# Kernel optimization log

Hardware: AMD Instinct MI355X
Metric: run time of the kernel (lower is better)

The kernel has to match this reference:

```python
import jax, jax.numpy as jnp
import numpy as np

N, M, KNN, KUP, POS_DIM = 15872, 35637, 5, 20, 32


def _pos_emb_table(n, d):
    # transformer-style sinusoidal table (matches PosEmb._define_pos_emb)
    pos = np.arange(n, dtype=np.float32)[:, None]
    i2 = np.arange(0, d, 2, dtype=np.float32)
    div = 10000.0 ** (i2 / d)
    pe = np.zeros((n, d), dtype=np.float32)
    pe[:, 0::2] = np.sin(pos / div)
    pe[:, 1::2] = np.cos(pos / div)
    return jnp.asarray(pe)


def _lrelu(x):
    return jnp.where(x > 0, x, 0.2 * x)


def _gather(x, idx):
    # x: [B,n,d], idx: [B,m,k] -> [B,m,k,d]
    return jax.vmap(lambda xb, ib: xb[ib])(x, idx)


def _knn_idx(x, k):
    # x: [B,n,d]; k nearest excluding self (torch knn drops column 0 of topk)
    xx = jnp.sum(x * x, axis=-1)
    neg = 2.0 * jnp.einsum('bnd,bmd->bnm', x, x) - xx[:, :, None] - xx[:, None, :]
    _, idx = jax.lax.top_k(neg, k + 1)
    return idx[..., 1:]


def _emb_block(feat, idx, ec_w1, ec_s1, ec_h1, ec_w2, ec_b2,
               w1, s1, h1, w2, s2, h2, w3, s3, h3, w4, b4):
    # get_graph_feature: [B,n,k,2*in] = cat(nbr - ctr, ctr)
    nbr = _gather(feat, idx)
    ctr = jnp.broadcast_to(feat[:, :, None, :], nbr.shape)
    e = jnp.concatenate([nbr - ctr, ctr], axis=-1)
    # edge_conv (1x1 conv2d = per-edge linear); BN folded into scale/shift (eval mode)
    e = _lrelu(jnp.einsum('bnkc,oc->bnko', e, ec_w1) * ec_s1 + ec_h1)
    e = jnp.einsum('bnkc,oc->bnko', e, ec_w2) + ec_b2
    f1 = jnp.max(e, axis=2)                                   # max over k neighbors -> [B,n,out]
    fmax = jnp.broadcast_to(jnp.max(f1, axis=1, keepdims=True), f1.shape)
    favg = jnp.broadcast_to(jnp.mean(f1, axis=1, keepdims=True), f1.shape)
    h = jnp.concatenate([feat, f1, fmax, favg], axis=-1)      # [B,n,3*out+in]
    # fc_out: 1x1 conv1d stack = per-point MLP with folded BN + LeakyReLU
    h = _lrelu(h @ w1.T * s1 + h1)
    h = _lrelu(h @ w2.T * s2 + h2)
    h = _lrelu(h @ w3.T * s3 + h3)
    return h @ w4.T + b4


def _forward(lx, ldx, pos_emb,
             b0_ec_w1, b0_ec_s1, b0_ec_h1, b0_ec_w2, b0_ec_b2,
             b0_fc_w1, b0_fc_s1, b0_fc_h1, b0_fc_w2, b0_fc_s2, b0_fc_h2,
             b0_fc_w3, b0_fc_s3, b0_fc_h3, b0_fc_w4, b0_fc_b4,
             b1_ec_w1, b1_ec_s1, b1_ec_h1, b1_ec_w2, b1_ec_b2,
             b1_fc_w1, b1_fc_s1, b1_fc_h1, b1_fc_w2, b1_fc_s2, b1_fc_h2,
             b1_fc_w3, b1_fc_s3, b1_fc_h3, b1_fc_w4, b1_fc_b4,
             up_inputs, up_w0, up_s0, up_h0, up_w_rest, up_s_rest, up_h_rest, up_wf, up_bf,
             dec_w0, dec_b0, dec_w1, dec_b1, dec_w2, dec_b2, dec_w3, dec_b3,
             dec_w4, dec_b4, dec_wf, dec_bf,
             idx0, up_idx):
    B = ldx.shape[0]
    feat_in = jnp.concatenate([ldx, jnp.broadcast_to(pos_emb[None], (B,) + pos_emb.shape)], axis=-1)  # [B,N,35]
    f0 = _emb_block(feat_in, idx0,
                    b0_ec_w1, b0_ec_s1, b0_ec_h1, b0_ec_w2, b0_ec_b2,
                    b0_fc_w1, b0_fc_s1, b0_fc_h1, b0_fc_w2, b0_fc_s2, b0_fc_h2,
                    b0_fc_w3, b0_fc_s3, b0_fc_h3, b0_fc_w4, b0_fc_b4)   # [B,N,64]
    idx1 = _knn_idx(f0, KNN)                                            # dynamic feature-space KNN
    f1 = _emb_block(f0, idx1,
                    b1_ec_w1, b1_ec_s1, b1_ec_h1, b1_ec_w2, b1_ec_b2,
                    b1_fc_w1, b1_fc_s1, b1_fc_h1, b1_fc_w2, b1_fc_s2, b1_fc_h2,
                    b1_fc_w3, b1_fc_s3, b1_fc_h3, b1_fc_w4, b1_fc_b4)   # [B,N,128]
    x_feat = jnp.concatenate([feat_in, f0, f1], axis=-1)                # [B,N,227]
    # Upscale: SIREN-activated 1x1-conv stack -> softmax interpolation weights over KUP lo-res nbrs
    h = jnp.sin(jnp.einsum('bmkc,oc->bmko', up_inputs[:B], up_w0) * up_s0 + up_h0)
    for i in range(up_w_rest.shape[0]):
        h = jnp.sin(jnp.einsum('bmkc,oc->bmko', h, up_w_rest[i]) * up_s_rest[i] + up_h_rest[i])
    logits = jnp.einsum('bmkc,oc->bmko', h, up_wf) + up_bf              # [B,M,KUP,1]
    w = jax.nn.softmax(logits, axis=2)
    grouped = _gather(x_feat, up_idx)                                   # [B,M,KUP,227]
    z = jnp.sum(w * grouped, axis=2)                                    # [B,M,227]
    # SIREN decoder: dims [227,256,128,64,32,16,3]; zip with 5 mods applies first 5 layers + head
    h = jnp.sin(30.0 * (z @ dec_w0.T + dec_b0))
    h = jnp.sin(h @ dec_w1.T + dec_b1)
    h = jnp.sin(h @ dec_w2.T + dec_b2)
    h = jnp.sin(h @ dec_w3.T + dec_b3)
    h = jnp.sin(h @ dec_w4.T + dec_b4)
    return h @ dec_wf.T + dec_bf                                        # [B,M,3]


def setup_inputs():
    key = jax.random.key(0)
    ks = iter(jax.random.split(key, 100))
    def rn(*s):
        return jax.random.normal(next(ks), s, jnp.float32) * 0.05
    def sc(*s):
        return jax.random.uniform(next(ks), s, jnp.float32, minval=0.5, maxval=1.5)
    inp = {}
    inp['lx'] = jax.random.normal(next(ks), (1, N, 3), jnp.float32)
    inp['ldx'] = jax.random.normal(next(ks), (1, N, 3), jnp.float32)
    inp['pos_emb'] = _pos_emb_table(N, POS_DIM)
    inp['idx0'] = jax.random.randint(next(ks), (1, N, KNN), 0, N - 1)
    # EmbModule 0: in=35, out=64
    inp['b0_ec_w1'], inp['b0_ec_s1'], inp['b0_ec_h1'] = rn(128, 70), sc(128), rn(128)
    inp['b0_ec_w2'], inp['b0_ec_b2'] = rn(64, 128), rn(64)
    inp['b0_fc_w1'], inp['b0_fc_s1'], inp['b0_fc_h1'] = rn(192, 227), sc(192), rn(192)
    inp['b0_fc_w2'], inp['b0_fc_s2'], inp['b0_fc_h2'] = rn(128, 192), sc(128), rn(128)
    inp['b0_fc_w3'], inp['b0_fc_s3'], inp['b0_fc_h3'] = rn(64, 128), sc(64), rn(64)
    inp['b0_fc_w4'], inp['b0_fc_b4'] = rn(64, 64), rn(64)
    # EmbModule 1: in=64, out=128
    inp['b1_ec_w1'], inp['b1_ec_s1'], inp['b1_ec_h1'] = rn(256, 128), sc(256), rn(256)
    inp['b1_ec_w2'], inp['b1_ec_b2'] = rn(128, 256), rn(128)
    inp['b1_fc_w1'], inp['b1_fc_s1'], inp['b1_fc_h1'] = rn(384, 448), sc(384), rn(384)
    inp['b1_fc_w2'], inp['b1_fc_s2'], inp['b1_fc_h2'] = rn(256, 384), sc(256), rn(256)
    inp['b1_fc_w3'], inp['b1_fc_s3'], inp['b1_fc_h3'] = rn(128, 256), sc(128), rn(128)
    inp['b1_fc_w4'], inp['b1_fc_b4'] = rn(128, 128), rn(128)
    inp['up_inputs'] = jax.random.uniform(next(ks), (1, M, KUP, 7), jnp.float32)
    inp['up_idx'] = jax.random.randint(next(ks), (1, M, KUP), 0, N - 1)
    inp['up_w0'], inp['up_s0'], inp['up_h0'] = rn(128, 7), sc(128), rn(128)
    inp['up_w_rest'], inp['up_s_rest'], inp['up_h_rest'] = rn(7, 128, 128), sc(7, 128), rn(7, 128)
    inp['up_wf'], inp['up_bf'] = rn(1, 128), rn(1)
    # SIREN decoder
    dd = [227, 256, 128, 64, 32, 16]
    for i in range(5):
        inp['dec_w%d' % i], inp['dec_b%d' % i] = rn(dd[i + 1], dd[i]), rn(dd[i + 1])
    inp['dec_wf'], inp['dec_bf'] = rn(3, 16), rn(3)
    return inp


def reference(lx, ldx, pos_emb, idx0,
              b0_ec_w1, b0_ec_s1, b0_ec_h1, b0_ec_w2, b0_ec_b2,
              b0_fc_w1, b0_fc_s1, b0_fc_h1, b0_fc_w2, b0_fc_s2, b0_fc_h2,
              b0_fc_w3, b0_fc_s3, b0_fc_h3, b0_fc_w4, b0_fc_b4,
              b1_ec_w1, b1_ec_s1, b1_ec_h1, b1_ec_w2, b1_ec_b2,
              b1_fc_w1, b1_fc_s1, b1_fc_h1, b1_fc_w2, b1_fc_s2, b1_fc_h2,
              b1_fc_w3, b1_fc_s3, b1_fc_h3, b1_fc_w4, b1_fc_b4,
              up_inputs, up_idx, up_w0, up_s0, up_h0,
              up_w_rest, up_s_rest, up_h_rest, up_wf, up_bf,
              dec_w0, dec_b0, dec_w1, dec_b1, dec_w2, dec_b2, dec_w3, dec_b3,
              dec_w4, dec_b4, dec_wf, dec_bf):
    return _forward(lx, ldx, pos_emb,
                    b0_ec_w1, b0_ec_s1, b0_ec_h1, b0_ec_w2, b0_ec_b2,
                    b0_fc_w1, b0_fc_s1, b0_fc_h1, b0_fc_w2, b0_fc_s2, b0_fc_h2,
                    b0_fc_w3, b0_fc_s3, b0_fc_h3, b0_fc_w4, b0_fc_b4,
                    b1_ec_w1, b1_ec_s1, b1_ec_h1, b1_ec_w2, b1_ec_b2,
                    b1_fc_w1, b1_fc_s1, b1_fc_h1, b1_fc_w2, b1_fc_s2, b1_fc_h2,
                    b1_fc_w3, b1_fc_s3, b1_fc_h3, b1_fc_w4, b1_fc_b4,
                    up_inputs, up_w0, up_s0, up_h0, up_w_rest, up_s_rest, up_h_rest, up_wf, up_bf,
                    dec_w0, dec_b0, dec_w1, dec_b1, dec_w2, dec_b2, dec_w3, dec_b3,
                    dec_w4, dec_b4, dec_wf, dec_bf,
                    idx0, up_idx)
```

## Files before the change

kernel.cpp:

```cpp
#include <hip/hip_runtime.h>
#include <hip/hip_bf16.h>
#include <math.h>

#define N_PTS 15872
#define M_PTS 35637
#define KNN_K 5
#define KUP   20
#define UP_ROWS (M_PTS * KUP)
#define NTILE (N_PTS/32)
#define N_EDGE (N_PTS*KNN_K)
#define CDIV(a,b) (((a)+(b)-1)/(b))

typedef __hip_bfloat16 bf16;
typedef unsigned int uint;
typedef unsigned short ushort_t;
__device__ __forceinline__ float b2f(bf16 x){ return __bfloat162float(x); }

__device__ __forceinline__ uint f2bf_bits(float x){
  uint u = __float_as_uint(x);
  return (u + 0x7FFFu + ((u>>16)&1u)) >> 16;
}

__device__ __forceinline__ ushort_t f2h_bits(float x){
  union { _Float16 h; ushort_t u; } c; c.h = (_Float16)x; return c.u;
}

typedef __attribute__((ext_vector_type(8))) short bf16x8;
typedef __attribute__((ext_vector_type(8))) _Float16 f16x8;
typedef __attribute__((ext_vector_type(2))) __fp16 fp16x2_t;
typedef __attribute__((ext_vector_type(16))) float f32x16;
union FragAB { bf16x8 v; uint u[4]; };
union FragB  { bf16x8 v; uint4 q; };
union FragH  { f16x8 v; uint4 q; _Float16 h[8]; };
union Acc16  { f32x16 v; float f[16]; };
union H2U    { fp16x2_t h; uint u; };

__global__ void flag_k(const uint* __restrict__ pos_raw, int* __restrict__ flag){
  if (threadIdx.x == 0 && blockIdx.x == 0)
    flag[0] = (pos_raw[0] == 0x3F800000u) ? 1 : 0;
}

struct CvtTab { const void* src[52]; int start[52]; };
__global__ __launch_bounds__(256) void cvt_all_k(CvtTab tab, float* __restrict__ dst,
                                                 const int* __restrict__ flag, int total){
  int i = blockIdx.x*256 + threadIdx.x;
  if (i >= total) return;
  int s = 0;
#pragma unroll 1
  for (int k = 1; k < 52; k++) if (tab.start[k] <= i) s = k;
  int off = i - tab.start[s];
  float v = flag[0] ? b2f(((const bf16*)tab.src[s])[off]) : ((const float*)tab.src[s])[off];
  dst[i] = v;
}

__global__ void packfrag16_k(const float* __restrict__ w, const float* __restrict__ sr,
                             ushort_t* __restrict__ out, int n){
  int i = blockIdx.x*256 + threadIdx.x;
  if (i >= n) return;
  int j = i & 7;
  int lam = (i >> 3) & 63;
  int fg = i >> 9;
  int t = fg & 3, ks = (fg >> 2) & 1, Q = (fg >> 3) & 3, l = fg >> 5;
  int nn = t*32 + (lam & 31);
  int kk = Q*32 + ks*16 + ((j>>2)<<3) + ((lam>>5)<<2) + (j&3);
  float x = w[l*16384 + nn*128 + kk] * sr[l*128 + nn];
  out[i] = f2h_bits(x);
}

__global__ void packw_mfma_k(const float* __restrict__ w, ushort_t* __restrict__ whi,
                             ushort_t* __restrict__ wlo, int N, int K, int ldk,
                             int Kpad, int total){
  int i = blockIdx.x*256 + threadIdx.x;
  if (i >= total) return;
  int j = i & 7;
  int lane = (i >> 3) & 63;
  int fr = i >> 9;
  int nq = Kpad >> 5;
  int ks = fr & 1;
  int q  = (fr >> 1) % nq;
  int nt = (fr >> 1) / nq;
  int n = nt*32 + (lane & 31);
  int k = q*32 + ks*16 + (lane >> 5)*8 + j;
  float x = (n < N && k < K) ? w[(size_t)n*ldk + k] : 0.f;
  uint hb = f2bf_bits(x);
  uint lb = f2bf_bits(x - __uint_as_float(hb << 16));
  whi[i] = (ushort_t)hb;
  wlo[i] = (ushort_t)lb;
}

__global__ void packknn_k(const float* __restrict__ xf, const float* __restrict__ nr,
                          ushort_t* __restrict__ ahi, ushort_t* __restrict__ alo,
                          ushort_t* __restrict__ bhi, ushort_t* __restrict__ blo){
  int i = blockIdx.x*256 + threadIdx.x;
  if (i >= NTILE*5*64*8) return;
  int e = i & 7;
  int lane = (i >> 3) & 63;
  int rest = i >> 9;
  int kc = rest % 5, jt = rest / 5;
  int n = jt*32 + (lane & 31);
  int k = kc*16 + (lane >> 5)*8 + e;
  float f = (k < 64) ? xf[(size_t)n*227 + 35 + k] : 0.f;
  float av, bv;
  if (k < 64)      { av = 2.f*f;   bv = f; }
  else if (k == 64){ av = nr[n];   bv = -1.f; }
  else if (k == 65){ av = 1.f;     bv = -nr[n]; }
  else             { av = 0.f;     bv = 0.f; }
  uint ah = f2bf_bits(av); uint al = f2bf_bits(av - __uint_as_float(ah<<16));
  uint bh = f2bf_bits(bv); uint bl = f2bf_bits(bv - __uint_as_float(bh<<16));
  ahi[i] = (ushort_t)ah; alo[i] = (ushort_t)al;
  bhi[i] = (ushort_t)bh; blo[i] = (ushort_t)bl;
}

__global__ void fillmark_k(bf16* __restrict__ out, int n){
  int i = blockIdx.x*256 + threadIdx.x;
  if (i < n) out[i] = __float2bfloat16(12345.0f);
}

__global__ void foldshift_k(const float* __restrict__ W, int ldw,
                            int off1, int C1, const float* __restrict__ v1,
                            int off2, int C2, const float* __restrict__ v2,
                            const float* __restrict__ scale, const float* __restrict__ shift,
                            float* __restrict__ out, int N){
  int n = blockIdx.x*256 + threadIdx.x;
  if (n >= N) return;
  const float* wr = W + (size_t)n*ldw;
  float s = 0.f;
  for (int j=0;j<C1;j++) s += wr[off1+j]*v1[j];
  for (int j=0;j<C2;j++) s += wr[off2+j]*v2[j];
  out[n] = s*scale[n] + shift[n];
}

template<int EPI, int ACT>
__global__ __launch_bounds__(256) void gemm_k(
    const float* __restrict__ A, int lda,
    const float* __restrict__ W, int ldw,
    const float* __restrict__ scale, const float* __restrict__ shift,
    float gmul, float* __restrict__ C, int ldc,
    int M, int Nout, int K)
{
  __shared__ __align__(16) float As[16][64];
  __shared__ __align__(16) float Ws[16][64];
  const int tid = threadIdx.x;
  const int tx = tid & 15, ty = tid >> 4;
  const int bm = blockIdx.x * 64, bn = blockIdx.y * 64;
  const int ar = tid >> 2, ak = (tid & 3) * 4;
  float acc[4][4] = {};
  for (int k0 = 0; k0 < K; k0 += 16) {
    float a0=0.f,a1=0.f,a2=0.f,a3=0.f;
    int grow = bm + ar;
    if (grow < M) {
      const float* ap = A + (size_t)grow * lda + (k0 + ak);
      int rem = K - (k0 + ak);
      if (rem >= 4) { a0=ap[0]; a1=ap[1]; a2=ap[2]; a3=ap[3]; }
      else { if(rem>0)a0=ap[0]; if(rem>1)a1=ap[1]; if(rem>2)a2=ap[2]; }
    }
    float w0=0.f,w1=0.f,w2=0.f,w3=0.f;
    int gn = bn + ar;
    if (gn < Nout) {
      const float* wp = W + (size_t)gn * ldw + (k0 + ak);
      int rem = K - (k0 + ak);
      if (rem >= 4) { w0=wp[0]; w1=wp[1]; w2=wp[2]; w3=wp[3]; }
      else { if(rem>0)w0=wp[0]; if(rem>1)w1=wp[1]; if(rem>2)w2=wp[2]; }
    }
    __syncthreads();
    As[ak+0][ar]=a0; As[ak+1][ar]=a1; As[ak+2][ar]=a2; As[ak+3][ar]=a3;
    Ws[ak+0][ar]=w0; Ws[ak+1][ar]=w1; Ws[ak+2][ar]=w2; Ws[ak+3][ar]=w3;
    __syncthreads();
#pragma unroll
    for (int kk = 0; kk < 16; kk++) {
      float4 av = *reinterpret_cast<const float4*>(&As[kk][ty*4]);
      float4 wv = *reinterpret_cast<const float4*>(&Ws[kk][tx*4]);
      float aa[4] = {av.x,av.y,av.z,av.w};
      float ww[4] = {wv.x,wv.y,wv.z,wv.w};
#pragma unroll
      for (int i=0;i<4;i++)
#pragma unroll
        for (int j=0;j<4;j++) acc[i][j] += aa[i]*ww[j];
    }
  }
#pragma unroll
  for (int i=0;i<4;i++){
    int m = bm + ty*4 + i;
    if (m >= M) continue;
#pragma unroll
    for (int j=0;j<4;j++){
      int n = bn + tx*4 + j;
      if (n >= Nout) continue;
      float v = acc[i][j];
      if (EPI==0)      v = v * scale[n] + shift[n];
      else if (EPI==1) v = v + shift[n];
      else             v = (v + shift[n]) * gmul;
      if (ACT==1)      v = v > 0.f ? v : 0.2f*v;
      else if (ACT==2) v = sinf(v);
      C[(size_t)m*ldc + n] = v;
    }
  }
}

struct MLayer { int K, N, Kq, Nt, woff, soff, hoff, epi, act; float gmul; };
struct MCfg { MLayer L[6]; };

template<int NL, int OUTMODE>
__global__ __launch_bounds__(256) void mlp_fused_k(
    const float* __restrict__ A0, int lda0, int K0, int M,
    MCfg cfg,
    const ushort_t* __restrict__ wh, const ushort_t* __restrict__ wl,
    const float* __restrict__ wc,
    float* __restrict__ Cout, int ldc,
    void* __restrict__ oflg, const int* __restrict__ flag)
{
  __shared__ __align__(16) uint slab[64*256];
  const int tid = threadIdx.x;
  const int lane = tid & 63;
  const int wv = tid >> 6;
  const int np = lane & 31;
  const int hb2 = lane >> 5;
  const int rhalf = wv & 1, thalf = wv >> 1;
  const int rb = blockIdx.x * 64;
  const int row_l = rhalf*32 + np;

  for (int e = tid; e < 64*64; e += 256) {
    int r = e >> 6, g = e & 63;
    int gr = rb + r;
    uint p[4];
#pragma unroll
    for (int u=0;u<4;u++){
      int k = g*4+u;
      float f = (gr < M && k < K0) ? A0[(size_t)gr*lda0 + k] : 0.f;
      uint hb = f2bf_bits(f);
      uint lb = f2bf_bits(f - __uint_as_float(hb<<16));
      p[u] = (hb<<16) | lb;
    }
    *(uint4*)&slab[r*256 + (((g ^ r) & 63)<<2)] = make_uint4(p[0],p[1],p[2],p[3]);
  }
  __syncthreads();

#pragma unroll 1
  for (int l = 0; l < NL; l++){
    const int N = cfg.L[l].N, Kq = cfg.L[l].Kq, Nt = cfg.L[l].Nt;
    const int woff = cfg.L[l].woff, soff = cfg.L[l].soff, hoff = cfg.L[l].hoff;
    const int epi = cfg.L[l].epi, actf = cfg.L[l].act;
    const float gmul = cfg.L[l].gmul;
    Acc16 acc[4];
#pragma unroll
    for (int u=0;u<4;u++)
#pragma unroll
      for (int i=0;i<16;i++) acc[u].f[i] = 0.f;

#pragma unroll 1
    for (int q = 0; q < Kq; q++){
#pragma unroll
      for (int ks = 0; ks < 2; ks++){
        int g0 = (q*32 + ks*16 + hb2*8) >> 2;
        uint4 a0 = *(const uint4*)&slab[row_l*256 + ((((g0  ) ^ row_l) & 63)<<2)];
        uint4 a1 = *(const uint4*)&slab[row_l*256 + ((((g0+1) ^ row_l) & 63)<<2)];
        uint au[8] = {a0.x,a0.y,a0.z,a0.w,a1.x,a1.y,a1.z,a1.w};
        FragAB ah, al;
#pragma unroll
        for (int p=0;p<4;p++){
          ah.u[p] = (au[2*p]>>16)     | (au[2*p+1] & 0xFFFF0000u);
          al.u[p] = (au[2*p]&0xFFFFu) | (au[2*p+1]<<16);
        }
#pragma unroll
        for (int u=0;u<4;u++){
          int t = thalf + u*2;
          if (t < Nt){
            size_t fb = (size_t)woff + ((size_t)((t*Kq + q)*2 + ks))*512 + (size_t)lane*8;
            FragB bh, bl;
            bh.q = *(const uint4*)(wh + fb);
            bl.q = *(const uint4*)(wl + fb);
            acc[u].v = __builtin_amdgcn_mfma_f32_32x32x16_bf16(ah.v, bh.v, acc[u].v, 0,0,0);
            acc[u].v = __builtin_amdgcn_mfma_f32_32x32x16_bf16(al.v, bh.v, acc[u].v, 0,0,0);
            acc[u].v = __builtin_amdgcn_mfma_f32_32x32x16_bf16(ah.v, bl.v, acc[u].v, 0,0,0);
          }
        }
      }
    }
    __syncthreads();
#pragma unroll
    for (int u=0;u<4;u++){
      int t = thalf + u*2;
      if (t < Nt){
        int col = t*32 + np;
        if (col < N){
          float scv = (epi==0) ? wc[soff+col] : 0.f;
          float shv = wc[hoff+col];
#pragma unroll
          for (int reg=0;reg<16;reg++){
            int r32 = (reg&3) + 8*(reg>>2) + 4*hb2;
            float v = acc[u].f[reg];
            if (epi==0)      v = v*scv + shv;
            else if (epi==1) v = v + shv;
            else             v = (v + shv)*gmul;
            if (actf==1)      v = v > 0.f ? v : 0.2f*v;
            else if (actf==2) v = __sinf(v);
            if (l == NL-1){
              int gr = rb + rhalf*32 + r32;
              if (gr < M){
                if (OUTMODE==0) Cout[(size_t)gr*ldc + col] = v;
                else {
                  if (!(fabsf(v) < 1e30f)) v = 777.0f;
                  size_t oi = (size_t)gr*3 + col;
                  if (flag[0]) ((bf16*)oflg)[oi] = __float2bfloat16(v);
                  else         ((float*)oflg)[oi] = v;
                }
              }
            } else {
              int r = rhalf*32 + r32;
              uint hb = f2bf_bits(v);
              uint lb = f2bf_bits(v - __uint_as_float(hb<<16));
              slab[r*256 + ((((col>>2) ^ r) & 63)<<2) + (col&3)] = (hb<<16) | lb;
            }
          }
        }
      }
    }
    __syncthreads();
  }
}

#define INS5(tv, tj, v, j) \
  if ((v) > tv[4]){ tv[4]=(v); tj[4]=(j); \
    _Pragma("unroll") \
    for (int q=4;q>0;q--) \
      if (tv[q] > tv[q-1]){ float tf=tv[q-1]; tv[q-1]=tv[q]; tv[q]=tf; \
                            int ti=tj[q-1]; tj[q-1]=tj[q]; tj[q]=ti; } }

__global__ __launch_bounds__(256) void knn_mfma_k(
    const ushort_t* __restrict__ ahi, const ushort_t* __restrict__ alo,
    const ushort_t* __restrict__ bhi, const ushort_t* __restrict__ blo,
    int* __restrict__ out)
{
  __shared__ float mv[4][32][5];
  __shared__ int   mjj[4][32][5];
  const int tid = threadIdx.x;
  const int lane = tid & 63;
  const int wv = tid >> 6;
  const int np = lane & 31;
  const int hb2 = lane >> 5;
  const int it = blockIdx.x;
  const int ig = it*32 + np;

  FragB vh[5], vl[5];
  {
    size_t bb = (size_t)(it*5)*512 + (size_t)lane*8;
#pragma unroll
    for (int kc=0;kc<5;kc++){
      vh[kc].q = *(const uint4*)(bhi + bb + kc*512);
      vl[kc].q = *(const uint4*)(blo + bb + kc*512);
    }
  }

  float tv[5] = {-1e30f,-1e30f,-1e30f,-1e30f,-1e30f};
  int   tj[5] = {0,0,0,0,0};

  FragB uh[5], ul[5], nh[5], nl[5];
  {
    size_t ab = (size_t)(wv*5)*512 + (size_t)lane*8;
#pragma unroll
    for (int kc=0;kc<5;kc++){
      uh[kc].q = *(const uint4*)(ahi + ab + kc*512);
      ul[kc].q = *(const uint4*)(alo + ab + kc*512);
    }
  }

#pragma unroll 1
  for (int t = 0; t < NTILE/4; t++){
    int jt = wv + t*4;
    if (t+1 < NTILE/4){
      size_t an = (size_t)((jt+4)*5)*512 + (size_t)lane*8;
#pragma unroll
      for (int kc=0;kc<5;kc++){
        nh[kc].q = *(const uint4*)(ahi + an + kc*512);
        nl[kc].q = *(const uint4*)(alo + an + kc*512);
      }
    }
    Acc16 acc;
#pragma unroll
    for (int q=0;q<16;q++) acc.f[q] = 0.f;
#pragma unroll
    for (int kc=0;kc<5;kc++){
      acc.v = __builtin_amdgcn_mfma_f32_32x32x16_bf16(uh[kc].v, vh[kc].v, acc.v, 0,0,0);
      acc.v = __builtin_amdgcn_mfma_f32_32x32x16_bf16(ul[kc].v, vh[kc].v, acc.v, 0,0,0);
      acc.v = __builtin_amdgcn_mfma_f32_32x32x16_bf16(uh[kc].v, vl[kc].v, acc.v, 0,0,0);
    }
    int jb = jt*32 + 4*hb2;
#pragma unroll
    for (int reg=0;reg<16;reg++){
      int j = jb + (reg&3) + 8*(reg>>2);
      float v = acc.f[reg];
      if (j != ig) { INS5(tv, tj, v, j); }
    }
    if (t+1 < NTILE/4){
#pragma unroll
      for (int kc=0;kc<5;kc++){ uh[kc] = nh[kc]; ul[kc] = nl[kc]; }
    }
  }

#pragma unroll
  for (int s=0;s<5;s++){
    float ov = __shfl_xor(tv[s], 32, 64);
    int   oj = __shfl_xor(tj[s], 32, 64);
    INS5(tv, tj, ov, oj);
  }
  if (hb2 == 0){
#pragma unroll
    for (int s=0;s<5;s++){ mv[wv][np][s] = tv[s]; mjj[wv][np][s] = tj[s]; }
  }
  __syncthreads();
  if (tid < 32){
    float bv[5]; int bj[5];
#pragma unroll
    for (int s=0;s<5;s++){ bv[s] = mv[0][tid][s]; bj[s] = mjj[0][tid][s]; }
#pragma unroll
    for (int w=1;w<4;w++)
#pragma unroll
      for (int s=0;s<5;s++){
        float v = mv[w][tid][s]; int j = mjj[w][tid][s];
        INS5(bv, bj, v, j);
      }
    int gi = it*32 + tid;
#pragma unroll
    for (int s=0;s<5;s++) out[gi*KNN_K + s] = bj[s];
  }
}

__global__ __launch_bounds__(256) void siren_fused_k(
    const void* __restrict__ upin,
    const ushort_t* __restrict__ wf16,
    const float* __restrict__ W0c, const float* __restrict__ S0c, const float* __restrict__ H0c,
    const float* __restrict__ HRc,
    const float* __restrict__ WFc, const float* __restrict__ BFc,
    float* __restrict__ logits, const int* __restrict__ flag)
{
  __shared__ float intile[4*32*8];
  __shared__ __align__(16) float w0s[128*8];
  __shared__ __align__(16) float hrs[7*128];
  __shared__ __align__(16) float wfs[128];
  __shared__ float bfs[1];

  const int tid  = threadIdx.x;
  const int lane = tid & 63;
  const int wv   = tid >> 6;
  const int np   = lane & 31;
  const int hb2  = lane >> 5;
  const int rowbase = blockIdx.x * 128 + wv * 32;
  const int isbf = flag[0];
  float* intw = intile + wv*32*8;

  for (int e = tid; e < 128*7; e += 256){
    int c = e/7, k = e%7;
    w0s[c*8+k] = W0c[e]*S0c[c];
  }
  if (tid < 128) w0s[tid*8+7] = H0c[tid];
  for (int e = tid; e < 7*128; e += 256) hrs[e] = HRc[e];
  if (tid < 128) wfs[tid] = WFc[tid];
  if (tid == 0) bfs[0] = BFc[0];
  for (int e = lane; e < 32*7; e += 64) {
    int r = e/7, k = e%7;
    int gr = rowbase + r;
    float v = 0.f;
    if (gr < UP_ROWS)
      v = isbf ? b2f(((const bf16*)upin)[(size_t)gr*7+k]) : ((const float*)upin)[(size_t)gr*7+k];
    intw[r*8+k] = v;
  }
  __syncthreads();

  uint st0[16], st1[16];
  {
    float xin[7];
#pragma unroll
    for (int k=0;k<7;k++) xin[k] = intw[np*8+k];
#pragma unroll
    for (int g = 0; g < 16; g++){
      float xs[4];
#pragma unroll
      for (int j = 0; j < 4; j++){
        int c = g*8 + hb2*4 + j;
        const float4 wa = *(const float4*)&w0s[c*8];
        const float4 wb = *(const float4*)&w0s[c*8+4];
        float a = wb.w;
        a += xin[0]*wa.x; a += xin[1]*wa.y; a += xin[2]*wa.z; a += xin[3]*wa.w;
        a += xin[4]*wb.x; a += xin[5]*wb.y; a += xin[6]*wb.z;
        xs[j] = __sinf(a);
      }
      H2U u0,u1;
      u0.h = __builtin_amdgcn_cvt_pkrtz(xs[0],xs[1]);
      u1.h = __builtin_amdgcn_cvt_pkrtz(xs[2],xs[3]);
      st0[g] = u0.u; st1[g] = u1.u;
    }
  }

  FragH fr[8];
#pragma unroll
  for (int m = 0; m < 8; m++)
    fr[m].q = make_uint4(st0[2*m], st1[2*m], st0[2*m+1], st1[2*m+1]);

  uint nst0[16], nst1[16];
#pragma unroll 1
  for (int l = 0; l < 7; l++) {
#pragma unroll
    for (int tp = 0; tp < 2; tp++){
      Acc16 acc0, acc1;
#pragma unroll
      for (int i=0;i<16;i++){ acc0.f[i] = 0.f; acc1.f[i] = 0.f; }
#pragma unroll
      for (int m = 0; m < 8; m++){
        int fb = (((l*8 + m)*4 + tp*2) << 9) + lane*8;
        FragH bh0, bh1;
        bh0.q = *(const uint4*)(wf16 + fb);
        bh1.q = *(const uint4*)(wf16 + fb + 512);
        acc0.v = __builtin_amdgcn_mfma_f32_32x32x16_f16(bh0.v, fr[m].v, acc0.v, 0,0,0);
        acc1.v = __builtin_amdgcn_mfma_f32_32x32x16_f16(bh1.v, fr[m].v, acc1.v, 0,0,0);
      }
#pragma unroll
      for (int rg = 0; rg < 4; rg++){
        int g0 = (tp*2+0)*4 + rg;
        const float4 b0v = *(const float4*)&hrs[l*128 + g0*8 + hb2*4];
        float x0 = __sinf(acc0.f[rg*4+0] + b0v.x);
        float x1 = __sinf(acc0.f[rg*4+1] + b0v.y);
        float x2 = __sinf(acc0.f[rg*4+2] + b0v.z);
        float x3 = __sinf(acc0.f[rg*4+3] + b0v.w);
        H2U u0,u1;
        u0.h = __builtin_amdgcn_cvt_pkrtz(x0,x1);
        u1.h = __builtin_amdgcn_cvt_pkrtz(x2,x3);
        nst0[g0] = u0.u; nst1[g0] = u1.u;

        int g1 = (tp*2+1)*4 + rg;
        const float4 b1v = *(const float4*)&hrs[l*128 + g1*8 + hb2*4];
        float y0 = __sinf(acc1.f[rg*4+0] + b1v.x);
        float y1 = __sinf(acc1.f[rg*4+1] + b1v.y);
        float y2 = __sinf(acc1.f[rg*4+2] + b1v.z);
        float y3 = __sinf(acc1.f[rg*4+3] + b1v.w);
        H2U v0,v1;
        v0.h = __builtin_amdgcn_cvt_pkrtz(y0,y1);
        v1.h = __builtin_amdgcn_cvt_pkrtz(y2,y3);
        nst0[g1] = v0.u; nst1[g1] = v1.u;
      }
    }
    if (l < 6){
#pragma unroll
      for (int m = 0; m < 8; m++)
        fr[m].q = make_uint4(nst0[2*m], nst1[2*m], nst0[2*m+1], nst1[2*m+1]);
    }
  }

  {
    float a = 0.f;
#pragma unroll
    for (int g = 0; g < 16; g++){
      const float4 w4 = *(const float4*)&wfs[g*8 + hb2*4];
      H2U u0,u1; u0.u = nst0[g]; u1.u = nst1[g];
      a += (float)u0.h.x*w4.x + (float)u0.h.y*w4.y
         + (float)u1.h.x*w4.z + (float)u1.h.y*w4.w;
    }
    a += __shfl_xor(a, 32, 64);
    int gr = rowbase + np;
    if (hb2 == 0 && gr < UP_ROWS) logits[gr] = a + bfs[0];
  }
}

__global__ void featin_k(const void* __restrict__ ldx, const void* __restrict__ pos,
                         float* __restrict__ xf, const int* __restrict__ flag){
  int i = blockIdx.x*256 + threadIdx.x;
  if (i >= N_PTS*35) return;
  int n = i / 35, c = i % 35;
  float v;
  if (flag[0]) {
    v = (c < 3) ? b2f(((const bf16*)ldx)[n*3+c]) : b2f(((const bf16*)pos)[n*32 + (c-3)]);
  } else {
    v = (c < 3) ? ((const float*)ldx)[n*3+c] : ((const float*)pos)[n*32 + (c-3)];
  }
  xf[(size_t)n*227 + c] = v;
}

__global__ void gather_e_k(const float* __restrict__ xf, int coff, int CIN,
                           const int* __restrict__ idx, float* __restrict__ e,
                           int n0, int np){
  int W2 = 2*CIN;
  int i = blockIdx.x*256 + threadIdx.x;
  if (i >= np*KNN_K*W2) return;
  int c = i % W2; int ek = i / W2;
  int nl = ek / KNN_K, k = ek % KNN_K;
  int n = n0 + nl;
  int j = idx[n*KNN_K + k];
  float out;
  if (c < CIN) out = xf[(size_t)j*227 + coff + c] - xf[(size_t)n*227 + coff + c];
  else         out = xf[(size_t)n*227 + coff + (c-CIN)];
  e[(size_t)ek*W2 + c] = out;
}

__global__ void kmax_k(const float* __restrict__ e2, int C, float* __restrict__ f1,
                       int n0, int np){
  int i = blockIdx.x*256 + threadIdx.x;
  if (i >= np*C) return;
  int nl = i / C, c = i % C;
  float v = -1e30f;
  for (int k=0;k<KNN_K;k++) v = fmaxf(v, e2[((size_t)nl*KNN_K+k)*C + c]);
  f1[(size_t)(n0+nl)*C + c] = v;
}

template<int C>
__global__ __launch_bounds__(256) void reduce1_k(const float* __restrict__ X, int n,
                                                 float* __restrict__ pmax, float* __restrict__ psum){
  const int tid = threadIdx.x;
  const int c = tid % C;
  const int r0 = tid / C;
  const int TPR = 256 / C;
  float vmax = -1e30f, vsum = 0.f;
  for (int row = blockIdx.x * TPR + r0; row < n; row += gridDim.x * TPR) {
    float v = X[(size_t)row * C + c];
    vmax = fmaxf(vmax, v); vsum += v;
  }
  __shared__ float smax[256], ssum[256];
  smax[tid]=vmax; ssum[tid]=vsum;
  __syncthreads();
  if (tid < C) {
    for (int q=1;q<TPR;q++){ vmax=fmaxf(vmax, smax[q*C+c]); vsum += ssum[q*C+c]; }
    pmax[blockIdx.x*C + c] = vmax; psum[blockIdx.x*C + c] = vsum;
  }
}

template<int C>
__global__ void reduce2_k(const float* __restrict__ pmax, const float* __restrict__ psum,
                          int nblk, float invn, float* __restrict__ fmaxo, float* __restrict__ favgo){
  int c = threadIdx.x; if (c >= C) return;
  float vmax=-1e30f, vsum=0.f;
  for (int b=0;b<nblk;b++){ vmax=fmaxf(vmax,pmax[b*C+c]); vsum+=psum[b*C+c]; }
  fmaxo[c]=vmax; favgo[c]=vsum*invn;
}

__global__ void concat_k(const float* __restrict__ xf, int coff, int CF,
                         const float* __restrict__ f1, int C,
                         const float* __restrict__ fmax, const float* __restrict__ favg,
                         float* __restrict__ h, int n0, int np){
  int W = CF + 3*C;
  int i = blockIdx.x*256 + threadIdx.x;
  if (i >= np*W) return;
  int nl = i / W, c = i % W;
  int n = n0 + nl;
  float v;
  if (c < CF)          v = xf[(size_t)n*227 + coff + c];
  else if (c < CF+C)   v = f1[(size_t)n*C + (c-CF)];
  else if (c < CF+2*C) v = fmax[c-CF-C];
  else                 v = favg[c-CF-2*C];
  h[(size_t)nl*W + c] = v;
}

__global__ void concat2_k(const float* __restrict__ xf, int coff, int CF,
                          const float* __restrict__ f1, int C,
                          float* __restrict__ h, int n0, int np){
  int W = CF + C;
  int i = blockIdx.x*256 + threadIdx.x;
  if (i >= np*W) return;
  int nl = i / W, c = i % W;
  int n = n0 + nl;
  float v = (c < CF) ? xf[(size_t)n*227 + coff + c] : f1[(size_t)n*C + (c-CF)];
  h[(size_t)nl*W + c] = v;
}

__global__ void norms_k(const float* __restrict__ xf, float* __restrict__ nr){
  int n = blockIdx.x*256 + threadIdx.x;
  if (n >= N_PTS) return;
  const float* p = xf + (size_t)n*227 + 35;
  float s = 0.f;
  for (int d=0;d<64;d++) s += p[d]*p[d];
  nr[n] = s;
}

__global__ __launch_bounds__(64) void softgather_k(const float* __restrict__ logits,
                                                   const int* __restrict__ up_idx,
                                                   const float* __restrict__ xf,
                                                   float* __restrict__ z){
  __shared__ float lw[KUP]; __shared__ int li[KUP];
  int m = blockIdx.x;
  int tid = threadIdx.x;
  if (tid < KUP){ lw[tid] = logits[(size_t)m*KUP + tid]; li[tid] = up_idx[(size_t)m*KUP + tid]; }
  __syncthreads();
  float mx = -1e30f;
  for (int k=0;k<KUP;k++) mx = fmaxf(mx, lw[k]);
  __syncthreads();
  if (tid < KUP) lw[tid] = expf(lw[tid]-mx);
  __syncthreads();
  float s = 0.f;
  for (int k=0;k<KUP;k++) s += lw[k];
  float inv = 1.f/s;
  for (int c = tid; c < 227; c += 64){
    float acc = 0.f;
    for (int k=0;k<KUP;k++) acc += lw[k] * xf[(size_t)li[k]*227 + c];
    z[(size_t)m*227 + c] = acc*inv;
  }
}

extern "C" void kernel_launch(void* const* d_in, const int* in_sizes, int n_in,
                              void* d_out, int out_size, void* d_ws, size_t ws_size,
                              hipStream_t stream) {
  const int *idx0  = (const int*)d_in[3];
  const int *upidx = (const int*)d_in[37];

  float* ws = (float*)d_ws;
  float* x_feat = ws;
  float* f1b    = ws + 3602944;
  float* pmax   = ws + 5634560;
  float* psum   = ws + 5667328;
  float* fmaxv  = ws + 5700096;
  float* favgv  = ws + 5700224;
  int*   flag   = (int*)(ws + 5700352);
  int*   idx1   = (int*)(ws + 5700368);
  float* nrm    = ws + 5779728;
  float* logits = ws + 5795600;
  float* wcvt   = ws + 6508352;
  float* S      = ws + 7214400;
  float* fold0  = S + 9500000;
  float* fold1  = S + 9500192;
  ushort_t* whi  = (ushort_t*)(S + 9662464);
  ushort_t* wlo  = whi + 114688;
  ushort_t* gwhi = wlo + 114688;
  ushort_t* gwlo = gwhi + 331776;

  const size_t NEED = (size_t)(7214400 + 9662464) * 4
                    + (size_t)(114688*2 + 331776*2) * 2;
  if (ws_size < NEED) {
    fillmark_k<<<CDIV(out_size,256),256,0,stream>>>((bf16*)d_out, out_size);
    return;
  }

  flag_k<<<1,64,0,stream>>>((const uint*)d_in[2], flag);
  CvtTab tab;
  int wcoff = 0, seg = 0;
  auto CVT = [&](int i, int n)->const float* {
    tab.src[seg] = d_in[i]; tab.start[seg] = wcoff; seg++;
    const float* p = wcvt + wcoff; wcoff += n;
    return p;
  };
  const float *E0W1=CVT(4,8960),  *E0S1=CVT(5,128),  *E0H1=CVT(6,128),
              *E0W2=CVT(7,8192),  *E0B2=CVT(8,64);
  const float *F0W1=CVT(9,43584), *F0S1=CVT(10,192), *F0H1=CVT(11,192),
              *F0W2=CVT(12,24576),*F0S2=CVT(13,128), *F0H2=CVT(14,128),
              *F0W3=CVT(15,8192), *F0S3=CVT(16,64),  *F0H3=CVT(17,64),
              *F0W4=CVT(18,4096), *F0B4=CVT(19,64);
  const float *E1W1=CVT(20,32768),*E1S1=CVT(21,256), *E1H1=CVT(22,256),
              *E1W2=CVT(23,32768),*E1B2=CVT(24,128);
  const float *F1W1=CVT(25,172032),*F1S1=CVT(26,384),*F1H1=CVT(27,384),
              *F1W2=CVT(28,98304),*F1S2=CVT(29,256), *F1H2=CVT(30,256),
              *F1W3=CVT(31,32768),*F1S3=CVT(32,128), *F1H3=CVT(33,128),
              *F1W4=CVT(34,16384),*F1B4=CVT(35,128);
  const float *UPW0=CVT(38,896),  *UPS0=CVT(39,128), *UPH0=CVT(40,128),
              *UPWR=CVT(41,114688),*UPSR=CVT(42,896),*UPHR=CVT(43,896),
              *UPWF=CVT(44,128),  *UPBF=CVT(45,1);
  const float *DW0=CVT(46,58112), *DB0=CVT(47,256),
              *DW1=CVT(48,32768), *DB1=CVT(49,128),
              *DW2=CVT(50,8192),  *DB2=CVT(51,64),
              *DW3=CVT(52,2048),  *DB3=CVT(53,32),
              *DW4=CVT(54,512),   *DB4=CVT(55,16),
              *DWF=CVT(56,48),    *DBF=CVT(57,3);
  cvt_all_k<<<CDIV(wcoff,256),256,0,stream>>>(tab, wcvt, flag, wcoff);

  packfrag16_k<<<CDIV(114688,256),256,0,stream>>>(UPWR, UPSR, whi, 114688);

  int offs[16]; const float* srcs[16]; int Ns[16], Ks[16], Ldk[16], Kps[16];
  {
    int o = 0, q = 0;
    auto REG = [&](const float* s, int N, int K, int ldk, int Kpad){
      srcs[q]=s; Ns[q]=N; Ks[q]=K; Ldk[q]=ldk; Kps[q]=Kpad; offs[q]=o;
      o += CDIV(N,32)*32*Kpad; q++;
    };
    REG(F0W1,192, 99,227,128);
    REG(F0W2,128,192,192,192); REG(F0W3,64,128,128,128); REG(F0W4,64,64,64,64);
    REG(DW0,256,227,227,256);  REG(DW1,128,256,256,256);  REG(DW2,64,128,128,128);
    REG(DW3,32,64,64,64);      REG(DW4,16,32,32,32);      REG(DWF,3,16,16,32);
    REG(E0W1,128,70,70,96);    REG(E0W2,64,128,128,128);
    REG(E1W1,256,128,128,128); REG(E1W2,128,256,256,256);
    REG(F1W3,128,256,256,256); REG(F1W4,128,128,128,128);
  }
  for (int q = 0; q < 16; q++){
    int total = CDIV(Ns[q],32)*32*Kps[q];
    packw_mfma_k<<<CDIV(total,256),256,0,stream>>>(srcs[q], gwhi+offs[q], gwlo+offs[q],
                                                   Ns[q], Ks[q], Ldk[q], Kps[q], total);
  }

  auto OFF = [&](const float* p){ return (int)(p - wcvt); };
  const int HOFF0 = (int)(fold0 - wcvt);
  MCfg cfc0{};
  cfc0.L[0] = { 99,192,4,6, offs[0], OFF(F0S1), HOFF0,     0,1, 0.f};
  cfc0.L[1] = {192,128,6,4, offs[1], OFF(F0S2), OFF(F0H2), 0,1, 0.f};
  cfc0.L[2] = {128, 64,4,2, offs[2], OFF(F0S3), OFF(F0H3), 0,1, 0.f};
  cfc0.L[3] = { 64, 64,2,2, offs[3], 0,         OFF(F0B4), 1,0, 0.f};
  MCfg cdec{};
  cdec.L[0] = {227,256,8,8, offs[4], 0, OFF(DB0), 2,2, 30.f};
  cdec.L[1] = {256,128,8,4, offs[5], 0, OFF(DB1), 1,2, 0.f};
  cdec.L[2] = {128, 64,4,2, offs[6], 0, OFF(DB2), 1,2, 0.f};
  cdec.L[3] = { 64, 32,2,1, offs[7], 0, OFF(DB3), 1,2, 0.f};
  cdec.L[4] = { 32, 16,1,1, offs[8], 0, OFF(DB4), 1,2, 0.f};
  cdec.L[5] = { 16,  3,1,1, offs[9], 0, OFF(DBF), 1,0, 0.f};
  MCfg ce0{};
  ce0.L[0] = { 70,128,3,4, offs[10], OFF(E0S1), OFF(E0H1), 0,1, 0.f};
  ce0.L[1] = {128, 64,4,2, offs[11], 0,         OFF(E0B2), 1,0, 0.f};
  MCfg ce1{};
  ce1.L[0] = {128,256,4,8, offs[12], OFF(E1S1), OFF(E1H1), 0,1, 0.f};
  ce1.L[1] = {256,128,8,4, offs[13], 0,         OFF(E1B2), 1,0, 0.f};
  MCfg cf1t{};
  cf1t.L[0] = {256,128,8,4, offs[14], OFF(F1S3), OFF(F1H3), 0,1, 0.f};
  cf1t.L[1] = {128,128,4,4, offs[15], 0,         OFF(F1B4), 1,0, 0.f};

  const float invN = 1.f/(float)N_PTS;
  const int CHN = 8192;

  featin_k<<<CDIV(N_PTS*35,256),256,0,stream>>>(d_in[1], d_in[2], x_feat, flag);

  {
    const int P0 = N_PTS/2;
    for (int n0 = 0; n0 < N_PTS; n0 += P0) {
      int ne = P0 * KNN_K;
      float* eA   = S;
      float* eOut = S + 2777600;
      gather_e_k<<<CDIV(ne*70,256),256,0,stream>>>(x_feat, 0, 35, idx0, eA, n0, P0);
      mlp_fused_k<2,0><<<CDIV(ne,64),256,0,stream>>>(
          eA,70,70,ne, ce0, gwhi,gwlo,wcvt, eOut,64, nullptr, flag);
      kmax_k<<<CDIV(P0*64,256),256,0,stream>>>(eOut, 64, f1b, n0, P0);
    }
  }
  reduce1_k<64><<<256,256,0,stream>>>(f1b, N_PTS, pmax, psum);
  reduce2_k<64><<<1,64,0,stream>>>(pmax, psum, 256, invN, fmaxv, favgv);
  foldshift_k<<<1,256,0,stream>>>(F0W1,227, 99,64,fmaxv, 163,64,favgv,
                                  F0S1,F0H1, fold0, 192);
  {
    float* h = S;
    concat2_k<<<CDIV(N_PTS*99,256),256,0,stream>>>(x_feat,0,35, f1b,64, h, 0, N_PTS);
    mlp_fused_k<4,0><<<CDIV(N_PTS,64),256,0,stream>>>(
        h,99,99,N_PTS, cfc0, gwhi,gwlo,wcvt, x_feat+35,227, nullptr, flag);
  }

  norms_k<<<CDIV(N_PTS,256),256,0,stream>>>(x_feat, nrm);
  {
    const int PLANE = NTILE*5*64*8;
    ushort_t* ajhi = (ushort_t*)S;
    ushort_t* ajlo = ajhi + PLANE;
    ushort_t* bihi = ajlo + PLANE;
    ushort_t* bilo = bihi + PLANE;
    packknn_k<<<CDIV(PLANE,256),256,0,stream>>>(x_feat, nrm, ajhi, ajlo, bihi, bilo);
    knn_mfma_k<<<NTILE,256,0,stream>>>(ajhi, ajlo, bihi, bilo, idx1);
  }

  {
    const int P1 = 5952;
    for (int n0 = 0; n0 < N_PTS; n0 += P1) {
      int np = N_PTS - n0; if (np > P1) np = P1;
      int ne = np * KNN_K;
      float* eA   = S;
      float* eOut = S + 3809280;
      gather_e_k<<<CDIV(ne*128,256),256,0,stream>>>(x_feat, 35, 64, idx1, eA, n0, np);
      mlp_fused_k<2,0><<<CDIV(ne,64),256,0,stream>>>(
          eA,128,128,ne, ce1, gwhi,gwlo,wcvt, eOut,128, nullptr, flag);
      kmax_k<<<CDIV(np*128,256),256,0,stream>>>(eOut, 128, f1b, n0, np);
    }
  }
  reduce1_k<128><<<256,256,0,stream>>>(f1b, N_PTS, pmax, psum);
  reduce2_k<128><<<1,128,0,stream>>>(pmax, psum, 256, invN, fmaxv, favgv);
  foldshift_k<<<2,256,0,stream>>>(F1W1,448, 192,128,fmaxv, 320,128,favgv,
                                  F1S1,F1H1, fold1, 384);
  for (int n0 = 0; n0 < N_PTS; n0 += CHN) {
    int np = N_PTS - n0; if (np > CHN) np = CHN;
    float* h  = S;
    float* a1 = S + 3670016;
    int gx = CDIV(np,64);
    concat2_k<<<CDIV(np*192,256),256,0,stream>>>(x_feat,35,64, f1b,128, h, n0, np);
    gemm_k<0,1><<<dim3(gx,6),256,0,stream>>>(h,192,  F1W1,448, F1S1,fold1,0.f, a1,384, np,384,192);
    gemm_k<0,1><<<dim3(gx,4),256,0,stream>>>(a1,384, F1W2,384, F1S2,F1H2,0.f, h,256,  np,256,384);
    mlp_fused_k<2,0><<<gx,256,0,stream>>>(
        h,256,256,np, cf1t, gwhi,gwlo,wcvt, x_feat+(size_t)n0*227+99,227, nullptr, flag);
  }

  siren_fused_k<<<CDIV(UP_ROWS,128),256,0,stream>>>(
      d_in[36], whi, UPW0, UPS0, UPH0, UPHR, UPWF, UPBF, logits, flag);
  float* zbuf = S;
  softgather_k<<<M_PTS,64,0,stream>>>(logits, upidx, x_feat, zbuf);

  mlp_fused_k<6,1><<<CDIV(M_PTS,64),256,0,stream>>>(
      zbuf,227,227,M_PTS, cdec, gwhi,gwlo,wcvt, nullptr,0, d_out, flag);
}
```

Before: 2.045 ms.

## Merge weight packing, fuse reduce/fold kernels, drop chunking, batch softgather blocks

Replaces sixteen per-weight pack launches with one table-driven kernel and merges the reduce2 and foldshift kernels into a single launch. The edge-conv stage 0 now runs unchunked, and stage 1 runs in larger chunks, with the MLP writing its output in place over its input buffer. Softgather now handles four points per 256-thread block and keeps the softmax weights in registers. The aim is fewer launches and more work per block; the risk is the in-place MLP write, which is only safe if each block reads all of its input rows before writing.

```diff
diff --git a/kernel.cpp b/kernel.cpp
--- a/kernel.cpp
+++ b/kernel.cpp
@@ -67,21 +67,25 @@
   out[i] = f2h_bits(x);
 }
 
-__global__ void packw_mfma_k(const float* __restrict__ w, ushort_t* __restrict__ whi,
-                             ushort_t* __restrict__ wlo, int N, int K, int ldk,
-                             int Kpad, int total){
+struct PackTab { const float* src[16]; int N[16], K[16], ldk[16], Kpad[16], start[16]; };
+__global__ __launch_bounds__(256) void packw_all_k(PackTab t, ushort_t* __restrict__ whi,
+                                                   ushort_t* __restrict__ wlo, int total){
   int i = blockIdx.x*256 + threadIdx.x;
   if (i >= total) return;
-  int j = i & 7;
-  int lane = (i >> 3) & 63;
-  int fr = i >> 9;
-  int nq = Kpad >> 5;
+  int s = 0;
+#pragma unroll 1
+  for (int q = 1; q < 16; q++) if (t.start[q] <= i) s = q;
+  int ii = i - t.start[s];
+  int j = ii & 7;
+  int lane = (ii >> 3) & 63;
+  int fr = ii >> 9;
+  int nq = t.Kpad[s] >> 5;
   int ks = fr & 1;
   int q  = (fr >> 1) % nq;
   int nt = (fr >> 1) / nq;
   int n = nt*32 + (lane & 31);
   int k = q*32 + ks*16 + (lane >> 5)*8 + j;
-  float x = (n < N && k < K) ? w[(size_t)n*ldk + k] : 0.f;
+  float x = (n < t.N[s] && k < t.K[s]) ? t.src[s][(size_t)n*t.ldk[s] + k] : 0.f;
   uint hb = f2bf_bits(x);
   uint lb = f2bf_bits(x - __uint_as_float(hb << 16));
   whi[i] = (ushort_t)hb;
@@ -114,20 +118,6 @@
 __global__ void fillmark_k(bf16* __restrict__ out, int n){
   int i = blockIdx.x*256 + threadIdx.x;
   if (i < n) out[i] = __float2bfloat16(12345.0f);
-}
-
-__global__ void foldshift_k(const float* __restrict__ W, int ldw,
-                            int off1, int C1, const float* __restrict__ v1,
-                            int off2, int C2, const float* __restrict__ v2,
-                            const float* __restrict__ scale, const float* __restrict__ shift,
-                            float* __restrict__ out, int N){
-  int n = blockIdx.x*256 + threadIdx.x;
-  if (n >= N) return;
-  const float* wr = W + (size_t)n*ldw;
-  float s = 0.f;
-  for (int j=0;j<C1;j++) s += wr[off1+j]*v1[j];
-  for (int j=0;j<C2;j++) s += wr[off2+j]*v2[j];
-  out[n] = s*scale[n] + shift[n];
 }
 
 template<int EPI, int ACT>
@@ -590,13 +580,13 @@
   e[(size_t)ek*W2 + c] = out;
 }
 
-__global__ void kmax_k(const float* __restrict__ e2, int C, float* __restrict__ f1,
+__global__ void kmax_k(const float* __restrict__ e2, int C, int ld, float* __restrict__ f1,
                        int n0, int np){
   int i = blockIdx.x*256 + threadIdx.x;
   if (i >= np*C) return;
   int nl = i / C, c = i % C;
   float v = -1e30f;
-  for (int k=0;k<KNN_K;k++) v = fmaxf(v, e2[((size_t)nl*KNN_K+k)*C + c]);
+  for (int k=0;k<KNN_K;k++) v = fmaxf(v, e2[((size_t)nl*KNN_K+k)*ld + c]);
   f1[(size_t)(n0+nl)*C + c] = v;
 }
 
@@ -622,29 +612,28 @@
 }
 
 template<int C>
-__global__ void reduce2_k(const float* __restrict__ pmax, const float* __restrict__ psum,
-                          int nblk, float invn, float* __restrict__ fmaxo, float* __restrict__ favgo){
-  int c = threadIdx.x; if (c >= C) return;
-  float vmax=-1e30f, vsum=0.f;
-  for (int b=0;b<nblk;b++){ vmax=fmaxf(vmax,pmax[b*C+c]); vsum+=psum[b*C+c]; }
-  fmaxo[c]=vmax; favgo[c]=vsum*invn;
-}
-
-__global__ void concat_k(const float* __restrict__ xf, int coff, int CF,
-                         const float* __restrict__ f1, int C,
-                         const float* __restrict__ fmax, const float* __restrict__ favg,
-                         float* __restrict__ h, int n0, int np){
-  int W = CF + 3*C;
-  int i = blockIdx.x*256 + threadIdx.x;
-  if (i >= np*W) return;
-  int nl = i / W, c = i % W;
-  int n = n0 + nl;
-  float v;
-  if (c < CF)          v = xf[(size_t)n*227 + coff + c];
-  else if (c < CF+C)   v = f1[(size_t)n*C + (c-CF)];
-  else if (c < CF+2*C) v = fmax[c-CF-C];
-  else                 v = favg[c-CF-2*C];
-  h[(size_t)nl*W + c] = v;
+__global__ __launch_bounds__(256) void red2fold_k(
+    const float* __restrict__ pmax, const float* __restrict__ psum,
+    int nblk, float invn,
+    const float* __restrict__ W, int ldw, int off1, int off2,
+    const float* __restrict__ scale, const float* __restrict__ shift,
+    float* __restrict__ out, int N)
+{
+  __shared__ float smax[C], ssum[C];
+  int tid = threadIdx.x;
+  if (tid < C){
+    float vmax=-1e30f, vsum=0.f;
+    for (int b=0;b<nblk;b++){ vmax=fmaxf(vmax,pmax[b*C+tid]); vsum+=psum[b*C+tid]; }
+    smax[tid]=vmax; ssum[tid]=vsum*invn;
+  }
+  __syncthreads();
+  for (int n = tid; n < N; n += 256){
+    const float* wr = W + (size_t)n*ldw;
+    float s = 0.f;
+    for (int j=0;j<C;j++) s += wr[off1+j]*smax[j];
+    for (int j=0;j<C;j++) s += wr[off2+j]*ssum[j];
+    out[n] = s*scale[n] + shift[n];
+  }
 }
 
 __global__ void concat2_k(const float* __restrict__ xf, int coff, int CF,
@@ -668,27 +657,31 @@
   nr[n] = s;
 }
 
-__global__ __launch_bounds__(64) void softgather_k(const float* __restrict__ logits,
-                                                   const int* __restrict__ up_idx,
-                                                   const float* __restrict__ xf,
-                                                   float* __restrict__ z){
-  __shared__ float lw[KUP]; __shared__ int li[KUP];
-  int m = blockIdx.x;
-  int tid = threadIdx.x;
-  if (tid < KUP){ lw[tid] = logits[(size_t)m*KUP + tid]; li[tid] = up_idx[(size_t)m*KUP + tid]; }
+__global__ __launch_bounds__(256) void softgather_k(const float* __restrict__ logits,
+                                                    const int* __restrict__ up_idx,
+                                                    const float* __restrict__ xf,
+                                                    float* __restrict__ z){
+  __shared__ float lw[4][KUP]; __shared__ int li[4][KUP];
+  int sub = threadIdx.x >> 6;
+  int tid = threadIdx.x & 63;
+  int m = blockIdx.x*4 + sub;
+  bool ok = (m < M_PTS);
+  if (ok && tid < KUP){
+    lw[sub][tid] = logits[(size_t)m*KUP + tid];
+    li[sub][tid] = up_idx[(size_t)m*KUP + tid];
+  }
   __syncthreads();
-  float mx = -1e30f;
-  for (int k=0;k<KUP;k++) mx = fmaxf(mx, lw[k]);
-  __syncthreads();
-  if (tid < KUP) lw[tid] = expf(lw[tid]-mx);
-  __syncthreads();
-  float s = 0.f;
-  for (int k=0;k<KUP;k++) s += lw[k];
-  float inv = 1.f/s;
-  for (int c = tid; c < 227; c += 64){
-    float acc = 0.f;
-    for (int k=0;k<KUP;k++) acc += lw[k] * xf[(size_t)li[k]*227 + c];
-    z[(size_t)m*227 + c] = acc*inv;
+  if (ok){
+    float mx = -1e30f;
+    for (int k=0;k<KUP;k++) mx = fmaxf(mx, lw[sub][k]);
+    float w[KUP]; float s = 0.f;
+    for (int k=0;k<KUP;k++){ w[k] = expf(lw[sub][k]-mx); s += w[k]; }
+    float inv = 1.f/s;
+    for (int c = tid; c < 227; c += 64){
+      float acc = 0.f;
+      for (int k=0;k<KUP;k++) acc += w[k] * xf[(size_t)li[sub][k]*227 + c];
+      z[(size_t)m*227 + c] = acc*inv;
+    }
   }
 }
 
@@ -703,16 +696,14 @@
   float* f1b    = ws + 3602944;
   float* pmax   = ws + 5634560;
   float* psum   = ws + 5667328;
-  float* fmaxv  = ws + 5700096;
-  float* favgv  = ws + 5700224;
+  float* fold0  = pmax + 24576;
+  float* fold1  = psum + 24576;
   int*   flag   = (int*)(ws + 5700352);
   int*   idx1   = (int*)(ws + 5700368);
   float* nrm    = ws + 5779728;
   float* logits = ws + 5795600;
   float* wcvt   = ws + 6508352;
   float* S      = ws + 7214400;
-  float* fold0  = S + 9500000;
-  float* fold1  = S + 9500192;
   ushort_t* whi  = (ushort_t*)(S + 9662464);
   ushort_t* wlo  = whi + 114688;
   ushort_t* gwhi = wlo + 114688;
@@ -758,12 +749,15 @@
 
   packfrag16_k<<<CDIV(114688,256),256,0,stream>>>(UPWR, UPSR, whi, 114688);
 
-  int offs[16]; const float* srcs[16]; int Ns[16], Ks[16], Ldk[16], Kps[16];
+  PackTab ptab;
+  int offs[16];
+  int ptotal = 0;
   {
-    int o = 0, q = 0;
+    int q = 0;
     auto REG = [&](const float* s, int N, int K, int ldk, int Kpad){
-      srcs[q]=s; Ns[q]=N; Ks[q]=K; Ldk[q]=ldk; Kps[q]=Kpad; offs[q]=o;
-      o += CDIV(N,32)*32*Kpad; q++;
+      ptab.src[q]=s; ptab.N[q]=N; ptab.K[q]=K; ptab.ldk[q]=ldk; ptab.Kpad[q]=Kpad;
+      ptab.start[q]=ptotal; offs[q]=ptotal;
+      ptotal += CDIV(N,32)*32*Kpad; q++;
     };
     REG(F0W1,192, 99,227,128);
     REG(F0W2,128,192,192,192); REG(F0W3,64,128,128,128); REG(F0W4,64,64,64,64);
@@ -773,11 +767,7 @@
     REG(E1W1,256,128,128,128); REG(E1W2,128,256,256,256);
     REG(F1W3,128,256,256,256); REG(F1W4,128,128,128,128);
   }
-  for (int q = 0; q < 16; q++){
-    int total = CDIV(Ns[q],32)*32*Kps[q];
-    packw_mfma_k<<<CDIV(total,256),256,0,stream>>>(srcs[q], gwhi+offs[q], gwlo+offs[q],
-                                                   Ns[q], Ks[q], Ldk[q], Kps[q], total);
-  }
+  packw_all_k<<<CDIV(ptotal,256),256,0,stream>>>(ptab, gwhi, gwlo, ptotal);
 
   auto OFF = [&](const float* p){ return (int)(p - wcvt); };
   const int HOFF0 = (int)(fold0 - wcvt);
@@ -809,21 +799,15 @@
   featin_k<<<CDIV(N_PTS*35,256),256,0,stream>>>(d_in[1], d_in[2], x_feat, flag);
 
   {
-    const int P0 = N_PTS/2;
-    for (int n0 = 0; n0 < N_PTS; n0 += P0) {
-      int ne = P0 * KNN_K;
-      float* eA   = S;
-      float* eOut = S + 2777600;
-      gather_e_k<<<CDIV(ne*70,256),256,0,stream>>>(x_feat, 0, 35, idx0, eA, n0, P0);
-      mlp_fused_k<2,0><<<CDIV(ne,64),256,0,stream>>>(
-          eA,70,70,ne, ce0, gwhi,gwlo,wcvt, eOut,64, nullptr, flag);
-      kmax_k<<<CDIV(P0*64,256),256,0,stream>>>(eOut, 64, f1b, n0, P0);
-    }
+    float* eA = S;
+    gather_e_k<<<CDIV(N_EDGE*70,256),256,0,stream>>>(x_feat, 0, 35, idx0, eA, 0, N_PTS);
+    mlp_fused_k<2,0><<<CDIV(N_EDGE,64),256,0,stream>>>(
+        eA,70,70,N_EDGE, ce0, gwhi,gwlo,wcvt, eA,70, nullptr, flag);
+    kmax_k<<<CDIV(N_PTS*64,256),256,0,stream>>>(eA, 64, 70, f1b, 0, N_PTS);
   }
   reduce1_k<64><<<256,256,0,stream>>>(f1b, N_PTS, pmax, psum);
-  reduce2_k<64><<<1,64,0,stream>>>(pmax, psum, 256, invN, fmaxv, favgv);
-  foldshift_k<<<1,256,0,stream>>>(F0W1,227, 99,64,fmaxv, 163,64,favgv,
-                                  F0S1,F0H1, fold0, 192);
+  red2fold_k<64><<<1,256,0,stream>>>(pmax, psum, 256, invN,
+                                     F0W1,227, 99,163, F0S1,F0H1, fold0, 192);
   {
     float* h = S;
     concat2_k<<<CDIV(N_PTS*99,256),256,0,stream>>>(x_feat,0,35, f1b,64, h, 0, N_PTS);
@@ -843,22 +827,20 @@
   }
 
   {
-    const int P1 = 5952;
+    const int P1 = 7936;
     for (int n0 = 0; n0 < N_PTS; n0 += P1) {
       int np = N_PTS - n0; if (np > P1) np = P1;
       int ne = np * KNN_K;
-      float* eA   = S;
-      float* eOut = S + 3809280;
+      float* eA = S;
       gather_e_k<<<CDIV(ne*128,256),256,0,stream>>>(x_feat, 35, 64, idx1, eA, n0, np);
       mlp_fused_k<2,0><<<CDIV(ne,64),256,0,stream>>>(
-          eA,128,128,ne, ce1, gwhi,gwlo,wcvt, eOut,128, nullptr, flag);
-      kmax_k<<<CDIV(np*128,256),256,0,stream>>>(eOut, 128, f1b, n0, np);
+          eA,128,128,ne, ce1, gwhi,gwlo,wcvt, eA,128, nullptr, flag);
+      kmax_k<<<CDIV(np*128,256),256,0,stream>>>(eA, 128, 128, f1b, n0, np);
     }
   }
   reduce1_k<128><<<256,256,0,stream>>>(f1b, N_PTS, pmax, psum);
-  reduce2_k<128><<<1,128,0,stream>>>(pmax, psum, 256, invN, fmaxv, favgv);
-  foldshift_k<<<2,256,0,stream>>>(F1W1,448, 192,128,fmaxv, 320,128,favgv,
-                                  F1S1,F1H1, fold1, 384);
+  red2fold_k<128><<<1,256,0,stream>>>(pmax, psum, 256, invN,
+                                      F1W1,448, 192,320, F1S1,F1H1, fold1, 384);
   for (int n0 = 0; n0 < N_PTS; n0 += CHN) {
     int np = N_PTS - n0; if (np > CHN) np = CHN;
     float* h  = S;
@@ -874,7 +856,7 @@
   siren_fused_k<<<CDIV(UP_ROWS,128),256,0,stream>>>(
       d_in[36], whi, UPW0, UPS0, UPH0, UPHR, UPWF, UPBF, logits, flag);
   float* zbuf = S;
-  softgather_k<<<M_PTS,64,0,stream>>>(logits, upidx, x_feat, zbuf);
+  softgather_k<<<CDIV(M_PTS,4),256,0,stream>>>(logits, upidx, x_feat, zbuf);
 
   mlp_fused_k<6,1><<<CDIV(M_PTS,64),256,0,stream>>>(
       zbuf,227,227,M_PTS, cdec, gwhi,gwlo,wcvt, nullptr,0, d_out, flag);
```

New measurement: 1.847 ms. -9.7%, faster.
